# Kernel tuning notes

Measured on AMD Instinct MI355X. Metric: run time of the kernel, lower is better.

The kernel has to match this reference:

```python
import jax, jax.numpy as jnp
import numpy as np

N_TOKENS = 32768
D_MODEL = 4096
N_EXPERTS = 64


def setup_inputs() -> dict:
    key = jax.random.key(0)
    k1, k2 = jax.random.split(key)
    inputs = jax.random.normal(k1, (N_TOKENS, D_MODEL), dtype=jnp.float32)
    # nn.Linear default init scale ~ 1/sqrt(fan_in); keep scores well-conditioned
    W = jax.random.normal(k2, (N_EXPERTS, D_MODEL), dtype=jnp.float32) / np.sqrt(D_MODEL)
    b = jnp.zeros((N_EXPERTS,), dtype=jnp.float32)
    return {"inputs": inputs, "W": W, "b": b, "top_k": 2}


def reference(inputs, W, b, top_k):
    # scores: [N, E] = inputs @ W^T + b  (nn.Linear)
    scores = jnp.einsum('nd,ed->ne', inputs, W) + b
    # torch.topk(dim=1): top_k values (sorted descending) and their indices
    top_k_score, top_k_indices = jax.lax.top_k(scores, top_k)
    # softmax over the selected top_k scores only (dim=1)
    probabilities = jax.nn.softmax(top_k_score, axis=1)
    return probabilities, top_k_indices
```

## Files before the change

### kernel.cpp

```cpp
#include <hip/hip_runtime.h>
#include <math.h>

typedef short     s16x8 __attribute__((ext_vector_type(8)));
typedef unsigned short u16x4 __attribute__((ext_vector_type(4)));
typedef float     f32x4 __attribute__((ext_vector_type(4)));

#define M_TOKENS 32768
#define D_MODEL  4096
#define N_EXPERTS 64

constexpr int BT   = 64;
constexpr int BK   = 64;
constexpr int LROW = BK + 8;
constexpr int XSPL = BT * LROW;
constexpr int WSPL = N_EXPERTS * LROW;
constexpr int WSP_STRIDE = N_EXPERTS * D_MODEL;

__device__ __forceinline__ unsigned short f32_to_bf16(float f) {
    unsigned int u = __float_as_uint(f);
    u += 0x7fffu + ((u >> 16) & 1u);
    return (unsigned short)(u >> 16);
}
__device__ __forceinline__ float bf16_to_f32(unsigned short h) {
    return __uint_as_float(((unsigned int)h) << 16);
}

__global__ void split_w_kernel(const float* __restrict__ W, unsigned short* __restrict__ Wsp) {
    const int idx = blockIdx.x * 256 + threadIdx.x;
    const float v = W[idx];
    const unsigned short h0 = f32_to_bf16(v);
    const float r1 = v - bf16_to_f32(h0);
    const unsigned short h1 = f32_to_bf16(r1);
    const float r2 = r1 - bf16_to_f32(h1);
    const unsigned short h2 = f32_to_bf16(r2);
    Wsp[idx]                  = h0;
    Wsp[WSP_STRIDE + idx]     = h1;
    Wsp[2 * WSP_STRIDE + idx] = h2;
}

__global__ __launch_bounds__(128)
void router_mfma_kernel(const float* __restrict__ X,
                        const unsigned short* __restrict__ Wsp,
                        const float* __restrict__ b,
                        float* __restrict__ out)
{
    __shared__ __align__(16) unsigned short Xs[3 * XSPL];
    __shared__ __align__(16) unsigned short Ws[3 * WSPL];

    const int tid  = threadIdx.x;
    const int wv   = tid >> 6;
    const int lane = tid & 63;
    const int l15  = lane & 15;
    const int quad = lane >> 4;
    const int t0   = blockIdx.x * BT;

    f32x4 acc[2][4];
    f32x4 mst[2][4];
#pragma unroll
    for (int tt = 0; tt < 2; ++tt)
#pragma unroll
        for (int et = 0; et < 4; ++et) {
            acc[tt][et] = (f32x4){0.f, 0.f, 0.f, 0.f};
            mst[tt][et] = (f32x4){0.f, 0.f, 0.f, 0.f};
        }

    for (int k0 = 0; k0 < D_MODEL; k0 += BK) {
        __syncthreads();

#pragma unroll
        for (int i = 0; i < 8; ++i) {
            const int f   = tid + i * 128;
            const int row = f >> 4;
            const int col = (f & 15) << 2;
            const float4 xv = *reinterpret_cast<const float4*>(
                &X[(size_t)(t0 + row) * D_MODEL + k0 + col]);
            const float vv[4] = {xv.x, xv.y, xv.z, xv.w};
            u16x4 p0, p1, p2;
#pragma unroll
            for (int c = 0; c < 4; ++c) {
                const unsigned short h0 = f32_to_bf16(vv[c]);
                const float r1 = vv[c] - bf16_to_f32(h0);
                const unsigned short h1 = f32_to_bf16(r1);
                const float r2 = r1 - bf16_to_f32(h1);
                const unsigned short h2 = f32_to_bf16(r2);
                p0[c] = h0; p1[c] = h1; p2[c] = h2;
            }
            const int base = row * LROW + col;
            *reinterpret_cast<u16x4*>(&Xs[0 * XSPL + base]) = p0;
            *reinterpret_cast<u16x4*>(&Xs[1 * XSPL + base]) = p1;
            *reinterpret_cast<u16x4*>(&Xs[2 * XSPL + base]) = p2;
        }

#pragma unroll
        for (int i = 0; i < 12; ++i) {
            const int g   = tid + i * 128;
            const int s   = g >> 9;
            const int rem = g & 511;
            const int e   = rem >> 3;
            const int kq  = (rem & 7) << 3;
            const s16x8 w8 = *reinterpret_cast<const s16x8*>(
                &Wsp[(size_t)s * WSP_STRIDE + e * D_MODEL + k0 + kq]);
            *reinterpret_cast<s16x8*>(&Ws[s * WSPL + e * LROW + kq]) = w8;
        }
        __syncthreads();

#pragma unroll
        for (int ks = 0; ks < 2; ++ks) {
            s16x8 af[2][3];
#pragma unroll
            for (int tt = 0; tt < 2; ++tt) {
                const int row  = wv * 32 + tt * 16 + l15;
                const int koff = row * LROW + ks * 32 + quad * 8;
                af[tt][0] = *reinterpret_cast<const s16x8*>(&Xs[0 * XSPL + koff]);
                af[tt][1] = *reinterpret_cast<const s16x8*>(&Xs[1 * XSPL + koff]);
                af[tt][2] = *reinterpret_cast<const s16x8*>(&Xs[2 * XSPL + koff]);
            }
#pragma unroll
            for (int et = 0; et < 4; ++et) {
                const int erow = et * 16 + l15;
                const int koff = erow * LROW + ks * 32 + quad * 8;
                s16x8 bf[3];
                bf[0] = *reinterpret_cast<const s16x8*>(&Ws[0 * WSPL + koff]);
                bf[1] = *reinterpret_cast<const s16x8*>(&Ws[1 * WSPL + koff]);
                bf[2] = *reinterpret_cast<const s16x8*>(&Ws[2 * WSPL + koff]);
#pragma unroll
                for (int tt = 0; tt < 2; ++tt) {
                    f32x4 c = acc[tt][et];
                    c = __builtin_amdgcn_mfma_f32_16x16x32_bf16(af[tt][0], bf[0], c, 0, 0, 0);
                    c = __builtin_amdgcn_mfma_f32_16x16x32_bf16(af[tt][0], bf[1], c, 0, 0, 0);
                    c = __builtin_amdgcn_mfma_f32_16x16x32_bf16(af[tt][1], bf[0], c, 0, 0, 0);
                    c = __builtin_amdgcn_mfma_f32_16x16x32_bf16(af[tt][1], bf[1], c, 0, 0, 0);
                    c = __builtin_amdgcn_mfma_f32_16x16x32_bf16(af[tt][0], bf[2], c, 0, 0, 0);
                    c = __builtin_amdgcn_mfma_f32_16x16x32_bf16(af[tt][2], bf[0], c, 0, 0, 0);
                    acc[tt][et] = c;
                }
            }
        }

        if ((k0 >> 6) & 1) {
#pragma unroll
            for (int tt = 0; tt < 2; ++tt)
#pragma unroll
                for (int et = 0; et < 4; ++et) {
#pragma unroll
                    for (int r = 0; r < 4; ++r) mst[tt][et][r] += acc[tt][et][r];
                    acc[tt][et] = (f32x4){0.f, 0.f, 0.f, 0.f};
                }
        }
    }

    __syncthreads();
    float* Ss = reinterpret_cast<float*>(Xs);
#pragma unroll
    for (int tt = 0; tt < 2; ++tt)
#pragma unroll
        for (int et = 0; et < 4; ++et)
#pragma unroll
            for (int r = 0; r < 4; ++r) {
                const int tok = wv * 32 + tt * 16 + quad * 4 + r;
                const int e   = et * 16 + l15;
                Ss[tok * 65 + e] = mst[tt][et][r];
            }
    __syncthreads();

    if (tid < BT) {
        const int t = tid;
        float best = -INFINITY, second = -INFINITY;
        int bi = 0, si = 0;
        for (int e = 0; e < N_EXPERTS; ++e) {
            const float s = Ss[t * 65 + e] + b[e];
            if (s > best) {
                second = best; si = bi;
                best = s;      bi = e;
            } else if (s > second) {
                second = s;    si = e;
            }
        }
        const float e2 = expf(second - best);
        const float inv = 1.0f / (1.0f + e2);

        const size_t tg = (size_t)(t0 + t);
        out[tg * 2 + 0] = inv;
        out[tg * 2 + 1] = e2 * inv;
        float* idx_out = out + (size_t)M_TOKENS * 2;
        idx_out[tg * 2 + 0] = (float)bi;
        idx_out[tg * 2 + 1] = (float)si;
    }
}

extern "C" void kernel_launch(void* const* d_in, const int* in_sizes, int n_in,
                              void* d_out, int out_size, void* d_ws, size_t ws_size,
                              hipStream_t stream) {
    const float* X = (const float*)d_in[0];
    const float* W = (const float*)d_in[1];
    const float* b = (const float*)d_in[2];
    float* out = (float*)d_out;
    unsigned short* Wsp = (unsigned short*)d_ws;

    hipLaunchKernelGGL(split_w_kernel, dim3(WSP_STRIDE / 256), dim3(256), 0, stream, W, Wsp);
    hipLaunchKernelGGL(router_mfma_kernel, dim3(M_TOKENS / BT), dim3(128), 0, stream,
                       X, Wsp, b, out);
}
```

Measured before the change: 812.0 us.

## Switch to two-term fp16 split GEMM with register prefetch and swizzled LDS

Replaces the three-term bf16 split (6 MFMAs per tile) with a two-term scaled fp16 hi/lo split needing 3 MFMAs per tile, cutting matrix-core work in half. It also pre-swizzles W into chunk-contiguous planes, adds an XOR-swizzled LDS layout against bank conflicts, prefetches the next chunk's X and W into registers while computing, and moves to 256-thread blocks with a 2x2 wave tiling. The fp16 split with scaling carries range/precision risk for extreme values, which could flip top-k ties.

Result: faster. 726.5 us (-10.5%).

```diff
diff --git a/kernel.cpp b/kernel.cpp
--- a/kernel.cpp
+++ b/kernel.cpp
@@ -1,165 +1,166 @@
 #include <hip/hip_runtime.h>
 #include <math.h>
 
-typedef short     s16x8 __attribute__((ext_vector_type(8)));
-typedef unsigned short u16x4 __attribute__((ext_vector_type(4)));
-typedef float     f32x4 __attribute__((ext_vector_type(4)));
+typedef float    f32x4 __attribute__((ext_vector_type(4)));
+typedef _Float16 f16x8 __attribute__((ext_vector_type(8)));
+typedef _Float16 f16x4 __attribute__((ext_vector_type(4)));
 
 #define M_TOKENS 32768
 #define D_MODEL  4096
 #define N_EXPERTS 64
 
-constexpr int BT   = 64;
-constexpr int BK   = 64;
-constexpr int LROW = BK + 8;
-constexpr int XSPL = BT * LROW;
-constexpr int WSPL = N_EXPERTS * LROW;
-constexpr int WSP_STRIDE = N_EXPERTS * D_MODEL;
-
-__device__ __forceinline__ unsigned short f32_to_bf16(float f) {
-    unsigned int u = __float_as_uint(f);
-    u += 0x7fffu + ((u >> 16) & 1u);
-    return (unsigned short)(u >> 16);
+constexpr int BT = 64;
+constexpr int BK = 64;
+constexpr int NCHUNK = D_MODEL / BK;
+constexpr int PLANE  = N_EXPERTS * BK * 2;
+constexpr int CHUNK_BYTES = 2 * PLANE;
+constexpr float RS   = 2048.0f;
+constexpr float IRS  = 1.0f / 2048.0f;
+constexpr float WSC  = 64.0f;
+constexpr float IWSC = 1.0f / 64.0f;
+
+__global__ __launch_bounds__(256)
+void split_w_kernel(const float* __restrict__ W, unsigned char* __restrict__ Wsp)
+{
+    const int t = blockIdx.x * 256 + threadIdx.x;
+    const int e = t >> 9;
+    const int g = t & 511;
+    const int c = g >> 3;
+    const int q = g & 7;
+    const float* src = W + ((size_t)e << 12) + (c << 6) + (q << 3);
+    const float4 v0 = *reinterpret_cast<const float4*>(src);
+    const float4 v1 = *reinterpret_cast<const float4*>(src + 4);
+    const float vv[8] = {v0.x, v0.y, v0.z, v0.w, v1.x, v1.y, v1.z, v1.w};
+    f16x8 hv, lv;
+#pragma unroll
+    for (int j = 0; j < 8; ++j) {
+        const float s = vv[j] * WSC;
+        const _Float16 h = (_Float16)s;
+        const float r = (s - (float)h) * RS;
+        hv[j] = h;
+        lv[j] = (_Float16)r;
+    }
+    const int lin = e * 128 + q * 16;
+    const int sw  = lin ^ ((e & 7) << 4);
+    unsigned char* dst = Wsp + (size_t)c * CHUNK_BYTES + sw;
+    *reinterpret_cast<f16x8*>(dst)         = hv;
+    *reinterpret_cast<f16x8*>(dst + PLANE) = lv;
 }
-__device__ __forceinline__ float bf16_to_f32(unsigned short h) {
-    return __uint_as_float(((unsigned int)h) << 16);
-}
-
-__global__ void split_w_kernel(const float* __restrict__ W, unsigned short* __restrict__ Wsp) {
-    const int idx = blockIdx.x * 256 + threadIdx.x;
-    const float v = W[idx];
-    const unsigned short h0 = f32_to_bf16(v);
-    const float r1 = v - bf16_to_f32(h0);
-    const unsigned short h1 = f32_to_bf16(r1);
-    const float r2 = r1 - bf16_to_f32(h1);
-    const unsigned short h2 = f32_to_bf16(r2);
-    Wsp[idx]                  = h0;
-    Wsp[WSP_STRIDE + idx]     = h1;
-    Wsp[2 * WSP_STRIDE + idx] = h2;
-}
-
-__global__ __launch_bounds__(128)
+
+__global__ __launch_bounds__(256, 2)
 void router_mfma_kernel(const float* __restrict__ X,
-                        const unsigned short* __restrict__ Wsp,
+                        const unsigned char* __restrict__ Wsp,
                         const float* __restrict__ b,
                         float* __restrict__ out)
 {
-    __shared__ __align__(16) unsigned short Xs[3 * XSPL];
-    __shared__ __align__(16) unsigned short Ws[3 * WSPL];
+    __shared__ __align__(16) unsigned char SMEM[2 * CHUNK_BYTES];
+    unsigned char* Xs = SMEM;
+    unsigned char* Ws = SMEM + CHUNK_BYTES;
 
     const int tid  = threadIdx.x;
     const int wv   = tid >> 6;
     const int lane = tid & 63;
     const int l15  = lane & 15;
     const int quad = lane >> 4;
+    const int wr   = (wv >> 1) * 32;
+    const int wc   = (wv & 1) * 32;
     const int t0   = blockIdx.x * BT;
 
-    f32x4 acc[2][4];
-    f32x4 mst[2][4];
+    f32x4 a1[2][2], a2[2][2];
 #pragma unroll
     for (int tt = 0; tt < 2; ++tt)
 #pragma unroll
-        for (int et = 0; et < 4; ++et) {
-            acc[tt][et] = (f32x4){0.f, 0.f, 0.f, 0.f};
-            mst[tt][et] = (f32x4){0.f, 0.f, 0.f, 0.f};
-        }
-
-    for (int k0 = 0; k0 < D_MODEL; k0 += BK) {
+        for (int et = 0; et < 2; ++et) {
+            a1[tt][et] = (f32x4){0.f, 0.f, 0.f, 0.f};
+            a2[tt][et] = (f32x4){0.f, 0.f, 0.f, 0.f};
+        }
+
+    const int srow = tid >> 4;
+    const int scol = tid & 15;
+    const float* xptr = X + (size_t)(t0 + srow) * D_MODEL + (scol << 2);
+    const unsigned char* wptr = Wsp + tid * 16;
+
+    float4 xr[4];
+    f16x8  wrg[4];
+#pragma unroll
+    for (int i = 0; i < 4; ++i) {
+        xr[i]  = *reinterpret_cast<const float4*>(xptr + (size_t)i * 16 * D_MODEL);
+        wrg[i] = *reinterpret_cast<const f16x8*>(wptr + i * 4096);
+    }
+
+    for (int c = 0; c < NCHUNK; ++c) {
+        if (c) __syncthreads();
+
+#pragma unroll
+        for (int i = 0; i < 4; ++i) {
+            const float vv[4] = {xr[i].x, xr[i].y, xr[i].z, xr[i].w};
+            f16x4 hv, lv;
+#pragma unroll
+            for (int j = 0; j < 4; ++j) {
+                const _Float16 h = (_Float16)vv[j];
+                hv[j] = h;
+                lv[j] = (_Float16)((vv[j] - (float)h) * RS);
+            }
+            const int row = i * 16 + srow;
+            const int sw  = (row * 128 + (scol << 3)) ^ ((row & 7) << 4);
+            *reinterpret_cast<f16x4*>(Xs + sw)         = hv;
+            *reinterpret_cast<f16x4*>(Xs + PLANE + sw) = lv;
+        }
+#pragma unroll
+        for (int i = 0; i < 4; ++i)
+            *reinterpret_cast<f16x8*>(Ws + i * 4096 + tid * 16) = wrg[i];
+
         __syncthreads();
 
-#pragma unroll
-        for (int i = 0; i < 8; ++i) {
-            const int f   = tid + i * 128;
-            const int row = f >> 4;
-            const int col = (f & 15) << 2;
-            const float4 xv = *reinterpret_cast<const float4*>(
-                &X[(size_t)(t0 + row) * D_MODEL + k0 + col]);
-            const float vv[4] = {xv.x, xv.y, xv.z, xv.w};
-            u16x4 p0, p1, p2;
-#pragma unroll
-            for (int c = 0; c < 4; ++c) {
-                const unsigned short h0 = f32_to_bf16(vv[c]);
-                const float r1 = vv[c] - bf16_to_f32(h0);
-                const unsigned short h1 = f32_to_bf16(r1);
-                const float r2 = r1 - bf16_to_f32(h1);
-                const unsigned short h2 = f32_to_bf16(r2);
-                p0[c] = h0; p1[c] = h1; p2[c] = h2;
-            }
-            const int base = row * LROW + col;
-            *reinterpret_cast<u16x4*>(&Xs[0 * XSPL + base]) = p0;
-            *reinterpret_cast<u16x4*>(&Xs[1 * XSPL + base]) = p1;
-            *reinterpret_cast<u16x4*>(&Xs[2 * XSPL + base]) = p2;
-        }
-
-#pragma unroll
-        for (int i = 0; i < 12; ++i) {
-            const int g   = tid + i * 128;
-            const int s   = g >> 9;
-            const int rem = g & 511;
-            const int e   = rem >> 3;
-            const int kq  = (rem & 7) << 3;
-            const s16x8 w8 = *reinterpret_cast<const s16x8*>(
-                &Wsp[(size_t)s * WSP_STRIDE + e * D_MODEL + k0 + kq]);
-            *reinterpret_cast<s16x8*>(&Ws[s * WSPL + e * LROW + kq]) = w8;
-        }
-        __syncthreads();
+        if (c + 1 < NCHUNK) {
+            const float* xp = xptr + (c + 1) * BK;
+            const unsigned char* wp = wptr + (size_t)(c + 1) * CHUNK_BYTES;
+#pragma unroll
+            for (int i = 0; i < 4; ++i) {
+                xr[i]  = *reinterpret_cast<const float4*>(xp + (size_t)i * 16 * D_MODEL);
+                wrg[i] = *reinterpret_cast<const f16x8*>(wp + i * 4096);
+            }
+        }
 
 #pragma unroll
         for (int ks = 0; ks < 2; ++ks) {
-            s16x8 af[2][3];
+            f16x8 ah[2], al[2], bh[2], bl[2];
 #pragma unroll
             for (int tt = 0; tt < 2; ++tt) {
-                const int row  = wv * 32 + tt * 16 + l15;
-                const int koff = row * LROW + ks * 32 + quad * 8;
-                af[tt][0] = *reinterpret_cast<const s16x8*>(&Xs[0 * XSPL + koff]);
-                af[tt][1] = *reinterpret_cast<const s16x8*>(&Xs[1 * XSPL + koff]);
-                af[tt][2] = *reinterpret_cast<const s16x8*>(&Xs[2 * XSPL + koff]);
-            }
-#pragma unroll
-            for (int et = 0; et < 4; ++et) {
-                const int erow = et * 16 + l15;
-                const int koff = erow * LROW + ks * 32 + quad * 8;
-                s16x8 bf[3];
-                bf[0] = *reinterpret_cast<const s16x8*>(&Ws[0 * WSPL + koff]);
-                bf[1] = *reinterpret_cast<const s16x8*>(&Ws[1 * WSPL + koff]);
-                bf[2] = *reinterpret_cast<const s16x8*>(&Ws[2 * WSPL + koff]);
-#pragma unroll
-                for (int tt = 0; tt < 2; ++tt) {
-                    f32x4 c = acc[tt][et];
-                    c = __builtin_amdgcn_mfma_f32_16x16x32_bf16(af[tt][0], bf[0], c, 0, 0, 0);
-                    c = __builtin_amdgcn_mfma_f32_16x16x32_bf16(af[tt][0], bf[1], c, 0, 0, 0);
-                    c = __builtin_amdgcn_mfma_f32_16x16x32_bf16(af[tt][1], bf[0], c, 0, 0, 0);
-                    c = __builtin_amdgcn_mfma_f32_16x16x32_bf16(af[tt][1], bf[1], c, 0, 0, 0);
-                    c = __builtin_amdgcn_mfma_f32_16x16x32_bf16(af[tt][0], bf[2], c, 0, 0, 0);
-                    c = __builtin_amdgcn_mfma_f32_16x16x32_bf16(af[tt][2], bf[0], c, 0, 0, 0);
-                    acc[tt][et] = c;
+                const int row = wr + tt * 16 + l15;
+                const int sw  = (row * 128 + ks * 64 + quad * 16) ^ ((row & 7) << 4);
+                ah[tt] = *reinterpret_cast<const f16x8*>(Xs + sw);
+                al[tt] = *reinterpret_cast<const f16x8*>(Xs + PLANE + sw);
+            }
+#pragma unroll
+            for (int et = 0; et < 2; ++et) {
+                const int erow = wc + et * 16 + l15;
+                const int sw   = (erow * 128 + ks * 64 + quad * 16) ^ ((erow & 7) << 4);
+                bh[et] = *reinterpret_cast<const f16x8*>(Ws + sw);
+                bl[et] = *reinterpret_cast<const f16x8*>(Ws + PLANE + sw);
+            }
+#pragma unroll
+            for (int tt = 0; tt < 2; ++tt)
+#pragma unroll
+                for (int et = 0; et < 2; ++et) {
+                    a1[tt][et] = __builtin_amdgcn_mfma_f32_16x16x32_f16(ah[tt], bh[et], a1[tt][et], 0, 0, 0);
+                    a2[tt][et] = __builtin_amdgcn_mfma_f32_16x16x32_f16(ah[tt], bl[et], a2[tt][et], 0, 0, 0);
+                    a2[tt][et] = __builtin_amdgcn_mfma_f32_16x16x32_f16(al[tt], bh[et], a2[tt][et], 0, 0, 0);
                 }
-            }
-        }
-
-        if ((k0 >> 6) & 1) {
-#pragma unroll
-            for (int tt = 0; tt < 2; ++tt)
-#pragma unroll
-                for (int et = 0; et < 4; ++et) {
-#pragma unroll
-                    for (int r = 0; r < 4; ++r) mst[tt][et][r] += acc[tt][et][r];
-                    acc[tt][et] = (f32x4){0.f, 0.f, 0.f, 0.f};
-                }
         }
     }
 
     __syncthreads();
-    float* Ss = reinterpret_cast<float*>(Xs);
+    float* Ss = reinterpret_cast<float*>(SMEM);
 #pragma unroll
     for (int tt = 0; tt < 2; ++tt)
 #pragma unroll
-        for (int et = 0; et < 4; ++et)
+        for (int et = 0; et < 2; ++et)
 #pragma unroll
             for (int r = 0; r < 4; ++r) {
-                const int tok = wv * 32 + tt * 16 + quad * 4 + r;
-                const int e   = et * 16 + l15;
-                Ss[tok * 65 + e] = mst[tt][et][r];
+                const int tok = wr + tt * 16 + quad * 4 + r;
+                const int e   = wc + et * 16 + l15;
+                Ss[tok * 65 + e] = (a1[tt][et][r] + a2[tt][et][r] * IRS) * IWSC;
             }
     __syncthreads();
 
@@ -176,7 +177,7 @@
                 second = s;    si = e;
             }
         }
-        const float e2 = expf(second - best);
+        const float e2  = expf(second - best);
         const float inv = 1.0f / (1.0f + e2);
 
         const size_t tg = (size_t)(t0 + t);
@@ -195,9 +196,10 @@
     const float* W = (const float*)d_in[1];
     const float* b = (const float*)d_in[2];
     float* out = (float*)d_out;
-    unsigned short* Wsp = (unsigned short*)d_ws;
-
-    hipLaunchKernelGGL(split_w_kernel, dim3(WSP_STRIDE / 256), dim3(256), 0, stream, W, Wsp);
-    hipLaunchKernelGGL(router_mfma_kernel, dim3(M_TOKENS / BT), dim3(128), 0, stream,
+    unsigned char* Wsp = (unsigned char*)d_ws;
+
+    hipLaunchKernelGGL(split_w_kernel, dim3((N_EXPERTS * D_MODEL) / (256 * 8)), dim3(256), 0, stream,
+                       W, Wsp);
+    hipLaunchKernelGGL(router_mfma_kernel, dim3(M_TOKENS / BT), dim3(256), 0, stream,
                        X, Wsp, b, out);
 }
```
